# Performance work log

Hardware: AMD Instinct MI355X
Metric: run time of the kernel (lower is better)

The kernel has to match this reference:

```python
import jax, jax.numpy as jnp
import numpy as np

N_NODES = 20000
N_EDGES = 320000
D_IN = 512
D_OUT = 512


def setup_inputs() -> dict:
    key = jax.random.key(0)
    k1, k2, k3, k4, k5, k6 = jax.random.split(key, 6)
    stdv = 1.0 / np.sqrt(D_OUT)
    return {
        "h": jax.random.normal(k1, (N_NODES, D_IN), dtype=jnp.float32),
        "weight": jax.random.uniform(k2, (D_IN, D_OUT), dtype=jnp.float32, minval=-stdv, maxval=stdv),
        "bias": jax.random.uniform(k3, (D_OUT,), dtype=jnp.float32, minval=-stdv, maxval=stdv),
        # GCN symmetric normalization term per node (deg^{-1/2}); strictly positive
        "norm": jax.random.uniform(k4, (N_NODES, 1), dtype=jnp.float32, minval=0.05, maxval=1.0),
        "src": jax.random.randint(k5, (N_EDGES,), 0, N_NODES, dtype=jnp.int32),
        "dst": jax.random.randint(k6, (N_EDGES,), 0, N_NODES, dtype=jnp.int32),
    }


def reference(h, weight, bias, norm, src, dst):
    # dropout p=0 -> identity (eval mode)
    # pre-normalize after dense projection: [N, d_out]
    hw = norm * jnp.matmul(h, weight)
    # update_all(copy_u, sum): gather source features, scatter-sum into dst
    msg = hw[src]  # [E, d_out]
    agg = jax.ops.segment_sum(msg, dst, num_segments=N_NODES)  # [N, d_out]
    out = agg * norm + bias
    return jax.nn.relu(out)
```

## Files before the change

### kernel.cpp

```cpp
#include <hip/hip_runtime.h>

#define M_NODES 20000
#define N_EDGES_C 320000
#define DIM 512
#define MAX_DEG 64

typedef __attribute__((ext_vector_type(4))) float f32x4;
typedef __attribute__((ext_vector_type(2))) float f32x2;
typedef __attribute__((ext_vector_type(4))) __bf16 bf16x4;
typedef __attribute__((ext_vector_type(8))) __bf16 bf16x8;

__device__ __forceinline__ void async16(__bf16* lds, const __bf16* g) {
  __builtin_amdgcn_global_load_lds(
      (const __attribute__((address_space(1))) void*)g,
      (__attribute__((address_space(3))) void*)lds, 16, 0, 0);
}

__global__ __launch_bounds__(256) void zero_k(int4* __restrict__ cnt4) {
  const int i = blockIdx.x * 256 + threadIdx.x;
  if (i < M_NODES / 4) cnt4[i] = int4{0, 0, 0, 0};
}

__global__ __launch_bounds__(256) void pre_k(const float* __restrict__ h,
                                             const float* __restrict__ w,
                                             const float* __restrict__ norm,
                                             const int* __restrict__ src,
                                             const int* __restrict__ dst,
                                             __bf16* __restrict__ hb,
                                             __bf16* __restrict__ wT,
                                             int* __restrict__ cnt,
                                             int* __restrict__ esrc) {
  const int bid = blockIdx.x;
  const int tid = threadIdx.x;
  const int gtid = bid * 256 + tid;
  const int gsz = gridDim.x * 256;

  const int nunits = (M_NODES / 32) * 8;
  for (int u = bid; u < nunits; u += gridDim.x) {
    const int p = u & 7;
    const int row = (u >> 3) * 32 + (tid >> 3);
    const int col = p * 64 + (tid & 7) * 8;
    const float s = norm[row];
    const float* hp = &h[(size_t)row * DIM + col];
    f32x4 v0 = *(const f32x4*)hp;
    f32x4 v1 = *(const f32x4*)(hp + 4);
    bf16x8 o;
    o[0] = (__bf16)(v0.x * s); o[1] = (__bf16)(v0.y * s);
    o[2] = (__bf16)(v0.z * s); o[3] = (__bf16)(v0.w * s);
    o[4] = (__bf16)(v1.x * s); o[5] = (__bf16)(v1.y * s);
    o[6] = (__bf16)(v1.z * s); o[7] = (__bf16)(v1.w * s);
    *(bf16x8*)&hb[(size_t)row * DIM + col] = o;
  }

  if (bid < 256) {
    __shared__ float tile[32][33];
    const int bx = (bid & 15) * 32, by = (bid >> 4) * 32;
    const int tx = tid & 31, ty8 = tid >> 5;
#pragma unroll
    for (int st = 0; st < 4; ++st) {
      const int r = ty8 + st * 8;
      tile[r][tx] = w[(by + r) * DIM + bx + tx];
    }
    __syncthreads();
#pragma unroll
    for (int st = 0; st < 4; ++st) {
      const int r = ty8 + st * 8;
      wT[(bx + r) * DIM + by + tx] = (__bf16)tile[tx][r];
    }
  }

  for (int e = gtid; e < N_EDGES_C; e += gsz) {
    const int d = dst[e];
    const int p = atomicAdd(&cnt[d], 1);
    if (p < MAX_DEG) esrc[d * MAX_DEG + p] = src[e];
  }
}

__global__ __launch_bounds__(256) void aggregate_k(const __bf16* __restrict__ hb,
                                                   const int* __restrict__ cnt,
                                                   const int* __restrict__ esrc,
                                                   __bf16* __restrict__ aggb) {
  const int panel = blockIdx.x & 7;
  const int nb = blockIdx.x >> 3;
  const int wv = threadIdx.x >> 6;
  const int lane = threadIdx.x & 63;
  const int slot = lane >> 3;
  const int cg = lane & 7;
  const int node = nb * 32 + wv * 8 + slot;

  const int beg = node * MAX_DEG;
  const int end = beg + cnt[node];
  const size_t pbase = (size_t)panel * 64 + cg * 8;

  f32x2 a2[4] = {};
  int j = beg;
  while (j + 8 <= end) {
    const int idx = esrc[j + cg];
    int sid[8];
#pragma unroll
    for (int g = 0; g < 8; ++g) sid[g] = __shfl(idx, (lane & 56) + g, 64);
#pragma unroll
    for (int g = 0; g < 8; ++g) {
      const uint4 u = *(const uint4*)&hb[(size_t)sid[g] * DIM + pbase];
      f32x2 p0 = {__uint_as_float(u.x << 16), __uint_as_float(u.x & 0xFFFF0000u)};
      f32x2 p1 = {__uint_as_float(u.y << 16), __uint_as_float(u.y & 0xFFFF0000u)};
      f32x2 p2 = {__uint_as_float(u.z << 16), __uint_as_float(u.z & 0xFFFF0000u)};
      f32x2 p3 = {__uint_as_float(u.w << 16), __uint_as_float(u.w & 0xFFFF0000u)};
      a2[0] += p0; a2[1] += p1; a2[2] += p2; a2[3] += p3;
    }
    j += 8;
  }
  for (; j < end; ++j) {
    const uint4 u = *(const uint4*)&hb[(size_t)esrc[j] * DIM + pbase];
    f32x2 p0 = {__uint_as_float(u.x << 16), __uint_as_float(u.x & 0xFFFF0000u)};
    f32x2 p1 = {__uint_as_float(u.y << 16), __uint_as_float(u.y & 0xFFFF0000u)};
    f32x2 p2 = {__uint_as_float(u.z << 16), __uint_as_float(u.z & 0xFFFF0000u)};
    f32x2 p3 = {__uint_as_float(u.w << 16), __uint_as_float(u.w & 0xFFFF0000u)};
    a2[0] += p0; a2[1] += p1; a2[2] += p2; a2[3] += p3;
  }
  bf16x8 o;
#pragma unroll
  for (int q = 0; q < 4; ++q) {
    o[2 * q]     = (__bf16)a2[q].x;
    o[2 * q + 1] = (__bf16)a2[q].y;
  }
  *(bf16x8*)&aggb[(size_t)node * DIM + pbase] = o;
}

__global__ __launch_bounds__(256, 2) void gemm_k(const __bf16* __restrict__ A,
                                                 const __bf16* __restrict__ B,
                                                 const float* __restrict__ bias,
                                                 const float* __restrict__ norm,
                                                 float* __restrict__ C) {
  __shared__ __bf16 As[3][64 * 64];
  __shared__ __bf16 Bs[3][128 * 64];
  const int tid = threadIdx.x;
  const int lane = tid & 63;
  const int wv = tid >> 6;
  const int wr = wv >> 1, wc = wv & 1;
  const int m0 = blockIdx.x * 64;
  const int n0 = blockIdx.y * 128;

  f32x4 acc[2][4] = {};

  const int srow = tid >> 3;
  const int scol = ((tid & 7) ^ (srow & 7)) * 8;
  const int ldst = (tid & 7) * 8;

  auto stage = [&](int buf, int kt) {
    const int kb = kt * 64 + scol;
#pragma unroll
    for (int jj = 0; jj < 2; ++jj) {
      const int lrow = jj * 32 + srow;
      int arow = m0 + lrow;
      arow = arow < M_NODES ? arow : (M_NODES - 1);
      async16(&As[buf][lrow * 64 + ldst], A + (size_t)arow * DIM + kb);
    }
#pragma unroll
    for (int jj = 0; jj < 4; ++jj) {
      const int lrow = jj * 32 + srow;
      async16(&Bs[buf][lrow * 64 + ldst], B + (size_t)(n0 + lrow) * DIM + kb);
    }
  };

  stage(0, 0);
  stage(1, 1);

  int cb = 0;
  for (int kt = 0; kt < DIM / 64; ++kt) {
    if (kt < DIM / 64 - 1)
      asm volatile("s_waitcnt vmcnt(6)" ::: "memory");
    else
      asm volatile("s_waitcnt vmcnt(0)" ::: "memory");
    __builtin_amdgcn_s_barrier();
    asm volatile("" ::: "memory");

    if (kt + 2 < DIM / 64) {
      int sb = cb + 2; if (sb >= 3) sb -= 3;
      stage(sb, kt + 2);
    }

#pragma unroll
    for (int kk = 0; kk < 64; kk += 32) {
      const int c = (kk >> 3) + (lane >> 4);
      bf16x8 af[2], bfr[4];
#pragma unroll
      for (int m = 0; m < 2; ++m) {
        const int r = wr * 32 + m * 16 + (lane & 15);
        af[m] = *(const bf16x8*)&As[cb][r * 64 + ((c ^ (r & 7)) * 8)];
      }
#pragma unroll
      for (int n = 0; n < 4; ++n) {
        const int r = wc * 64 + n * 16 + (lane & 15);
        bfr[n] = *(const bf16x8*)&Bs[cb][r * 64 + ((c ^ (r & 7)) * 8)];
      }
#pragma unroll
      for (int m = 0; m < 2; ++m)
#pragma unroll
        for (int n = 0; n < 4; ++n)
          acc[m][n] = __builtin_amdgcn_mfma_f32_16x16x32_bf16(af[m], bfr[n], acc[m][n], 0, 0, 0);
    }
    cb = (cb == 2) ? 0 : cb + 1;
  }

#pragma unroll
  for (int m = 0; m < 2; ++m) {
    const int rbase = m0 + wr * 32 + m * 16 + (lane >> 4) * 4;
#pragma unroll
    for (int r = 0; r < 4; ++r) {
      const int row = rbase + r;
      if (row < M_NODES) {
        const float nv = norm[row];
#pragma unroll
        for (int n = 0; n < 4; ++n) {
          const int col = n0 + wc * 64 + n * 16 + (lane & 15);
          float v = acc[m][n][r] * nv + bias[col];
          C[(size_t)row * DIM + col] = v > 0.f ? v : 0.f;
        }
      }
    }
  }
}

#define HB_OFF   0UL
#define AGG_OFF  20480000UL
#define WT_OFF   40960000UL
#define CNT_OFF  41484288UL
#define ESRC_OFF 41564288UL
#define WS_NEEDED 46684288UL

extern "C" void kernel_launch(void* const* d_in, const int* in_sizes, int n_in,
                              void* d_out, int out_size, void* d_ws, size_t ws_size,
                              hipStream_t stream) {
  const float* h    = (const float*)d_in[0];
  const float* w    = (const float*)d_in[1];
  const float* bias = (const float*)d_in[2];
  const float* norm = (const float*)d_in[3];
  const int*   src  = (const int*)d_in[4];
  const int*   dst  = (const int*)d_in[5];
  float* out = (float*)d_out;

  if (ws_size < WS_NEEDED) return;

  char* ws = (char*)d_ws;
  __bf16* hb   = (__bf16*)(ws + HB_OFF);
  __bf16* aggb = (__bf16*)(ws + AGG_OFF);
  __bf16* wT   = (__bf16*)(ws + WT_OFF);
  int*    cnt  = (int*)(ws + CNT_OFF);
  int*    esrc = (int*)(ws + ESRC_OFF);

  zero_k<<<20, 256, 0, stream>>>((int4*)cnt);
  pre_k<<<2048, 256, 0, stream>>>(h, w, norm, src, dst, hb, wT, cnt, esrc);
  aggregate_k<<<5000, 256, 0, stream>>>(hb, cnt, esrc, aggb);
  gemm_k<<<dim3(313, 4), 256, 0, stream>>>(aggb, wT, bias, norm, out);
}
```

Measured before the change: 98.52 us.

## Keep full-K weight tile resident in LDS and stream smaller A tiles in GEMM

The GEMM now loads the block's entire 128x512 bf16 weight slice into LDS once (128 KB) and streams only 32-row A tiles through a triple buffer. The M tile shrinks from 64 to 32, doubling the grid, and each wave owns a 32-column strip. This removes the per-k-step weight reloads and barriers on B, but the large LDS footprint limits residency to one block per CU. It also raises the weight-load overhead per output row, since each block now covers half as many rows.

```diff
diff --git a/kernel.cpp b/kernel.cpp
--- a/kernel.cpp
+++ b/kernel.cpp
@@ -127,96 +127,92 @@
   *(bf16x8*)&aggb[(size_t)node * DIM + pbase] = o;
 }
 
-__global__ __launch_bounds__(256, 2) void gemm_k(const __bf16* __restrict__ A,
+__global__ __launch_bounds__(256, 1) void gemm_k(const __bf16* __restrict__ A,
                                                  const __bf16* __restrict__ B,
                                                  const float* __restrict__ bias,
                                                  const float* __restrict__ norm,
                                                  float* __restrict__ C) {
-  __shared__ __bf16 As[3][64 * 64];
-  __shared__ __bf16 Bs[3][128 * 64];
+  __shared__ __bf16 Bs[128 * 512];
+  __shared__ __bf16 As[3][32 * 64];
   const int tid = threadIdx.x;
   const int lane = tid & 63;
   const int wv = tid >> 6;
-  const int wr = wv >> 1, wc = wv & 1;
-  const int m0 = blockIdx.x * 64;
+  const int m0 = blockIdx.x * 32;
   const int n0 = blockIdx.y * 128;
 
-  f32x4 acc[2][4] = {};
-
-  const int srow = tid >> 3;
-  const int scol = ((tid & 7) ^ (srow & 7)) * 8;
-  const int ldst = (tid & 7) * 8;
-
-  auto stage = [&](int buf, int kt) {
-    const int kb = kt * 64 + scol;
-#pragma unroll
-    for (int jj = 0; jj < 2; ++jj) {
-      const int lrow = jj * 32 + srow;
-      int arow = m0 + lrow;
-      arow = arow < M_NODES ? arow : (M_NODES - 1);
-      async16(&As[buf][lrow * 64 + ldst], A + (size_t)arow * DIM + kb);
-    }
-#pragma unroll
-    for (int jj = 0; jj < 4; ++jj) {
-      const int lrow = jj * 32 + srow;
-      async16(&Bs[buf][lrow * 64 + ldst], B + (size_t)(n0 + lrow) * DIM + kb);
-    }
+#pragma unroll
+  for (int p = 0; p < 32; ++p) {
+    const int u = p * 256 + tid;
+    const int r = u >> 6;
+    const int c = u & 63;
+    const int g = c ^ (r & 7);
+    async16(&Bs[r * 512 + c * 8], B + (size_t)(n0 + r) * DIM + g * 8);
+  }
+
+  auto stageA = [&](int buf, int kt) {
+    const int r = tid >> 3;
+    const int c = tid & 7;
+    const int g = c ^ (r & 7);
+    async16(&As[buf][r * 64 + c * 8],
+            A + (size_t)(m0 + r) * DIM + kt * 64 + g * 8);
   };
 
-  stage(0, 0);
-  stage(1, 1);
-
-  int cb = 0;
-  for (int kt = 0; kt < DIM / 64; ++kt) {
-    if (kt < DIM / 64 - 1)
-      asm volatile("s_waitcnt vmcnt(6)" ::: "memory");
-    else
-      asm volatile("s_waitcnt vmcnt(0)" ::: "memory");
-    __builtin_amdgcn_s_barrier();
-    asm volatile("" ::: "memory");
-
-    if (kt + 2 < DIM / 64) {
-      int sb = cb + 2; if (sb >= 3) sb -= 3;
-      stage(sb, kt + 2);
-    }
+  stageA(0, 0);
+  stageA(1, 1);
+  asm volatile("s_waitcnt vmcnt(1)" ::: "memory");
+  __builtin_amdgcn_s_barrier();
+  asm volatile("" ::: "memory");
+
+  f32x4 acc[2][2] = {};
+
+  for (int kt = 0; kt < 8; ++kt) {
+    const int cb = kt % 3;
+    if (kt + 2 < 8) stageA((kt + 2) % 3, kt + 2);
 
 #pragma unroll
     for (int kk = 0; kk < 64; kk += 32) {
-      const int c = (kk >> 3) + (lane >> 4);
-      bf16x8 af[2], bfr[4];
+      bf16x8 af[2], bf[2];
 #pragma unroll
       for (int m = 0; m < 2; ++m) {
-        const int r = wr * 32 + m * 16 + (lane & 15);
-        af[m] = *(const bf16x8*)&As[cb][r * 64 + ((c ^ (r & 7)) * 8)];
+        const int r = m * 16 + (lane & 15);
+        const int cp = (kk >> 3) + (lane >> 4);
+        af[m] = *(const bf16x8*)&As[cb][r * 64 + ((cp ^ (r & 7)) * 8)];
       }
 #pragma unroll
-      for (int n = 0; n < 4; ++n) {
-        const int r = wc * 64 + n * 16 + (lane & 15);
-        bfr[n] = *(const bf16x8*)&Bs[cb][r * 64 + ((c ^ (r & 7)) * 8)];
+      for (int n = 0; n < 2; ++n) {
+        const int rb = wv * 32 + n * 16 + (lane & 15);
+        const int cp = kt * 8 + (kk >> 3) + (lane >> 4);
+        bf[n] = *(const bf16x8*)&Bs[rb * 512 + ((cp ^ (rb & 7)) * 8)];
       }
 #pragma unroll
       for (int m = 0; m < 2; ++m)
 #pragma unroll
-        for (int n = 0; n < 4; ++n)
-          acc[m][n] = __builtin_amdgcn_mfma_f32_16x16x32_bf16(af[m], bfr[n], acc[m][n], 0, 0, 0);
-    }
-    cb = (cb == 2) ? 0 : cb + 1;
+        for (int n = 0; n < 2; ++n)
+          acc[m][n] = __builtin_amdgcn_mfma_f32_16x16x32_bf16(af[m], bf[n], acc[m][n], 0, 0, 0);
+    }
+
+    if (kt < 7) {
+      if (kt + 2 < 8)
+        asm volatile("s_waitcnt vmcnt(1)" ::: "memory");
+      else
+        asm volatile("s_waitcnt vmcnt(0)" ::: "memory");
+      __builtin_amdgcn_s_barrier();
+      asm volatile("" ::: "memory");
+    }
   }
 
 #pragma unroll
   for (int m = 0; m < 2; ++m) {
-    const int rbase = m0 + wr * 32 + m * 16 + (lane >> 4) * 4;
+    const int rbase = m0 + m * 16 + (lane >> 4) * 4;
 #pragma unroll
     for (int r = 0; r < 4; ++r) {
       const int row = rbase + r;
-      if (row < M_NODES) {
-        const float nv = norm[row];
-#pragma unroll
-        for (int n = 0; n < 4; ++n) {
-          const int col = n0 + wc * 64 + n * 16 + (lane & 15);
-          float v = acc[m][n][r] * nv + bias[col];
-          C[(size_t)row * DIM + col] = v > 0.f ? v : 0.f;
-        }
+      const float nv = norm[row];
+#pragma unroll
+      for (int n = 0; n < 2; ++n) {
+        const int col = n0 + wv * 32 + n * 16 + (lane & 15);
+        float v = acc[m][n][r] * nv + bias[col];
+        C[(size_t)row * DIM + col] = v > 0.f ? v : 0.f;
       }
     }
   }
@@ -252,5 +248,5 @@
   zero_k<<<20, 256, 0, stream>>>((int4*)cnt);
   pre_k<<<2048, 256, 0, stream>>>(h, w, norm, src, dst, hb, wT, cnt, esrc);
   aggregate_k<<<5000, 256, 0, stream>>>(hb, cnt, esrc, aggb);
-  gemm_k<<<dim3(313, 4), 256, 0, stream>>>(aggb, wT, bias, norm, out);
-}
+  gemm_k<<<dim3(625, 4), 256, 0, stream>>>(aggb, wT, bias, norm, out);
+}
```

New measurement: 114.7 us. 1.16x slower.
